# Optimization experiments

Measured on AMD Instinct MI355X. Metric: run time of the kernel, lower is better.

Reference implementation:

```python
import jax, jax.numpy as jnp
import numpy as np

NUM_EMB = 1024
EMB_DIM = 256
COMM_COST = 0.25
BETA = 0.25


def setup_inputs() -> dict:
    key = jax.random.key(0)
    k1, k2 = jax.random.split(key)
    x = jax.random.normal(k1, (16, EMB_DIM, 64, 64), dtype=jnp.float32)
    # nn.Embedding initialized uniform(-1/num_emb, 1/num_emb)
    emb_weight = jax.random.uniform(
        k2, (NUM_EMB, EMB_DIM), dtype=jnp.float32,
        minval=-1.0 / NUM_EMB, maxval=1.0 / NUM_EMB)
    return {"x": x, "emb_weight": emb_weight}


def reference(x, emb_weight):
    # x: [B, C, H, W] -> [B, H, W, C]
    xp = jnp.transpose(x, (0, 2, 3, 1))
    B, H, W, C = xp.shape
    flat = xp.reshape(-1, C)  # [N, C]
    # squared euclidean distances (argmin-equivalent to torch.cdist)
    d2 = (jnp.sum(flat * flat, axis=1, keepdims=True)
          - 2.0 * jnp.einsum('nc,kc->nk', flat, emb_weight)
          + jnp.sum(emb_weight * emb_weight, axis=1))  # [N, K]
    idx = jnp.argmin(d2, axis=1)  # [N]
    quantized = emb_weight[idx].reshape(B, H, W, C)
    e_latent_loss = jnp.mean((jax.lax.stop_gradient(quantized) - xp) ** 2) * BETA
    q_latent_loss = jnp.mean((quantized - jax.lax.stop_gradient(xp)) ** 2)
    c_loss = q_latent_loss + COMM_COST * e_latent_loss
    # straight-through estimator
    quant_st = xp + jax.lax.stop_gradient(quantized - xp)
    quant_out = jnp.transpose(quant_st, (0, 3, 1, 2))  # [B, C, H, W]
    return (c_loss, quant_out)
```

## Files before the change

### kernel.cpp

```cpp
#include <hip/hip_runtime.h>
#include <hip/hip_bf16.h>
#include <cstdint>
#include <cstddef>

#define EMB_K   1024
#define EMB_C   256
#define HWB     4096
#define NPIX    65536

typedef __bf16 bf16x8 __attribute__((ext_vector_type(8)));
typedef float  f32x4  __attribute__((ext_vector_type(4)));

__device__ __forceinline__ unsigned short bf16bits(float v) {
  __hip_bfloat16 h = __float2bfloat16(v);
  return __builtin_bit_cast(unsigned short, h);
}

__global__ void k_emb(const float* __restrict__ emb, unsigned short* __restrict__ emb_bf,
                      float* __restrict__ enorm, float* __restrict__ loss) {
  int k = blockIdx.x;
  int c = threadIdx.x;
  if (k == 0 && c == 0) *loss = 0.f;
  float v = emb[(size_t)k * EMB_C + c];
  emb_bf[(size_t)k * EMB_C + c] = bf16bits(v);
  float s = v * v;
  for (int m = 32; m; m >>= 1) s += __shfl_down(s, m, 64);
  __shared__ float red[4];
  int lane = c & 63, w = c >> 6;
  if (lane == 0) red[w] = s;
  __syncthreads();
  if (c == 0) enorm[k] = red[0] + red[1] + red[2] + red[3];
}

__global__ __launch_bounds__(512) void
k_tr(const float* __restrict__ x, unsigned short* __restrict__ A,
     float* __restrict__ xn_g) {
  __shared__ float xn_l[64];
  int t  = threadIdx.x;
  int n0 = blockIdx.x * 64;
  int b  = n0 >> 12, hw0 = n0 & 4095;
  int hwq = t & 15, c8 = t >> 4;
  if (t < 64) xn_l[t] = 0.f;
  __syncthreads();
  const float* xp = x + (size_t)b * (EMB_C * HWB) + hw0 + hwq * 4;
  float xn[4] = {0.f, 0.f, 0.f, 0.f};
  unsigned pk[4][4] = {};
#pragma unroll
  for (int j = 0; j < 8; ++j) {
    f32x4 v = *(const f32x4*)(xp + (size_t)(c8 * 8 + j) * HWB);
#pragma unroll
    for (int m = 0; m < 4; ++m) {
      xn[m] += v[m] * v[m];
      pk[m][j >> 1] |= (unsigned)bf16bits(v[m]) << ((j & 1) * 16);
    }
  }
  int s = c8 >> 2, quad = c8 & 3;
  uint4* A16 = (uint4*)A;
#pragma unroll
  for (int m = 0; m < 4; ++m) {
    int n  = n0 + hwq * 4 + m;
    int blk = n >> 8, nl = n & 255;
    int g = nl >> 6, i = (nl >> 4) & 3, lr = nl & 15;
    A16[(size_t)blk * 8192 + ((g * 4 + i) * 8 + s) * 64 + quad * 16 + lr]
        = *(const uint4*)pk[m];
    atomicAdd(&xn_l[hwq * 4 + m], xn[m]);
  }
  __syncthreads();
  if (t < 64) xn_g[n0 + t] = xn_l[t];
}

__device__ __forceinline__ void stage64(const unsigned short* __restrict__ rows,
                                        unsigned char* buf, int t) {
#pragma unroll
  for (int j = 0; j < 4; ++j) {
    int d = j * 512 + t;
    int r = d >> 5;
    int slot = d & 31;
    int c16 = ((slot >> 3) << 3) | ((slot & 7) ^ (r & 7));
    const unsigned short* src = rows + (size_t)r * EMB_C + c16 * 8;
    __builtin_amdgcn_global_load_lds(
        (const __attribute__((address_space(1))) void*)src,
        (__attribute__((address_space(3))) void*)(buf + (unsigned)(j * 8192 + (t >> 6) * 1024)),
        16, 0, 0);
  }
}

#define LDS_BYTES 137280

__global__ __launch_bounds__(512) void
k_main(const unsigned short* __restrict__ A, const unsigned short* __restrict__ embbf,
       const float* __restrict__ enorm, const float* __restrict__ xn_g,
       unsigned* __restrict__ keys_g, float* __restrict__ loss) {
  extern __shared__ char smem[];
  float*    cjl    = (float*)(smem + 131072);
  unsigned* keys_l = (unsigned*)(smem + 135168);
  float*    xn_l   = (float*)(smem + 136192);
  float*    red    = (float*)(smem + 137216);

  int n0 = blockIdx.x * 256;
  int t = threadIdx.x, w = t >> 6, lane = t & 63;
  int quad = lane >> 4, lr = lane & 15;
  int g  = w >> 1;
  int h2 = w & 1;

  stage64(embbf,               (unsigned char*)smem,         t);
  stage64(embbf + 64 * EMB_C,  (unsigned char*)smem + 32768, t);

  if (t < 256) { keys_l[t] = 0u; xn_l[t] = xn_g[n0 + t]; }
  for (int i = t; i < 1024; i += 512) cjl[i] = 0.375f - 0.5f * enorm[i];

  bf16x8 af[4][8];
  const uint4* Ab = (const uint4*)A + (size_t)blockIdx.x * 8192;
#pragma unroll
  for (int i = 0; i < 4; ++i)
#pragma unroll
    for (int s = 0; s < 8; ++s) {
      uint4 q = Ab[((g * 4 + i) * 8 + s) * 64 + lane];
      af[i][s] = __builtin_bit_cast(bf16x8, q);
    }
  __syncthreads();

  unsigned best[4][4] = {};
  for (int kt = 0; kt < 16; ++kt) {
    if (kt < 14)
      stage64(embbf + (size_t)(kt + 2) * 64 * EMB_C,
              (unsigned char*)smem + (((kt + 2) & 3) << 15), t);
    if (kt < 14)       asm volatile("s_waitcnt vmcnt(8)" ::: "memory");
    else if (kt == 14) asm volatile("s_waitcnt vmcnt(4)" ::: "memory");
    else               asm volatile("s_waitcnt vmcnt(0)" ::: "memory");
    __builtin_amdgcn_s_barrier();
    __builtin_amdgcn_sched_barrier(0);
    const unsigned char* srcB = (const unsigned char*)smem + ((kt & 3) << 15);
    float cj[2]; unsigned kp[2];
#pragma unroll
    for (int j = 0; j < 2; ++j) {
      int k = kt * 64 + h2 * 32 + j * 16 + lr;
      cj[j] = cjl[k];
      kp[j] = 1023u - (unsigned)k;
    }
    f32x4 acc[4][2] = {};
#pragma unroll
    for (int s = 0; s < 8; ++s) {
      int cc = s * 4 + quad;
      int pos = ((cc >> 3) << 3) | ((cc & 7) ^ (lr & 7));
      bf16x8 bf[2];
#pragma unroll
      for (int j = 0; j < 2; ++j)
        bf[j] = *(const bf16x8*)(srcB + (h2 * 32 + j * 16 + lr) * 512 + pos * 16);
#pragma unroll
      for (int i = 0; i < 4; ++i)
#pragma unroll
        for (int j = 0; j < 2; ++j)
          acc[i][j] = __builtin_amdgcn_mfma_f32_16x16x32_bf16(af[i][s], bf[j], acc[i][j], 0, 0, 0);
    }
#pragma unroll
    for (int i = 0; i < 4; ++i)
#pragma unroll
      for (int j = 0; j < 2; ++j)
#pragma unroll
        for (int r = 0; r < 4; ++r) {
          float f = acc[i][j][r] + cj[j];
          unsigned key = (__float_as_uint(f) & 0xFFFFFC00u) | kp[j];
          best[i][r] = best[i][r] > key ? best[i][r] : key;
        }
  }
  __syncthreads();

#pragma unroll
  for (int i = 0; i < 4; ++i)
#pragma unroll
    for (int r = 0; r < 4; ++r) {
      unsigned v = best[i][r];
#pragma unroll
      for (int m = 1; m < 16; m <<= 1) {
        unsigned o = (unsigned)__shfl_xor((int)v, m, 64);
        v = v > o ? v : o;
      }
      if (lr == 0) atomicMax(&keys_l[g * 64 + i * 16 + quad * 4 + r], v);
    }
  __syncthreads();

  if (t < 256) {
    unsigned key = keys_l[t];
    keys_g[n0 + t] = key;
    float fh = __uint_as_float(key & 0xFFFFFC00u);
    float lsum = xn_l[t] + 0.75f - 2.0f * fh;
    for (int m = 32; m; m >>= 1) lsum += __shfl_down(lsum, m, 64);
    if (lane == 0) red[w] = lsum;
  }
  __syncthreads();
  if (t == 0)
    atomicAdd(loss, red[0] + red[1] + red[2] + red[3]);
}

__global__ __launch_bounds__(256) void
k_out(const float* __restrict__ emb, const unsigned* __restrict__ keys_g,
      const float* __restrict__ loss, float* __restrict__ out) {
  __shared__ float tile[64 * 65];
  __shared__ int   idx_l[64];
  int e  = blockIdx.x;
  int nt = e >> 1, cH = e & 1;
  int n0 = nt * 64;
  int b  = n0 >> 12, hw0 = n0 & 4095;
  int t = threadIdx.x, w = t >> 6, lane = t & 63;
  if (e == 0 && t == 0)
    out[0] = 1.0625f * (*loss) / 16777216.0f;
  if (t < 64) idx_l[t] = 1023 - (int)(keys_g[n0 + t] & 1023u);
  __syncthreads();
  int nn = t >> 2, ch = t & 3;
  const float* er = emb + (size_t)idx_l[nn] * EMB_C + cH * 128;
  float* ob = out + 1 + (size_t)b * (EMB_C * HWB) + (size_t)cH * 128 * HWB + hw0;
  for (int p = 0; p < 2; ++p) {
    if (p) __syncthreads();
#pragma unroll
    for (int q = 0; q < 4; ++q) {
      f32x4 v = *(const f32x4*)(er + p * 64 + q * 16 + ch * 4);
#pragma unroll
      for (int m = 0; m < 4; ++m)
        tile[(q * 16 + ch * 4 + m) * 65 + nn] = v[m];
    }
    __syncthreads();
#pragma unroll
    for (int cc = 0; cc < 16; ++cc) {
      int cl = w * 16 + cc;
      ob[(size_t)(p * 64 + cl) * HWB + lane] = tile[cl * 65 + lane];
    }
  }
}

extern "C" void kernel_launch(void* const* d_in, const int* in_sizes, int n_in,
                              void* d_out, int out_size, void* d_ws, size_t ws_size,
                              hipStream_t stream) {
  const float* x   = (const float*)d_in[0];
  const float* emb = (const float*)d_in[1];
  float* out = (float*)d_out;
  char*  ws  = (char*)d_ws;

  unsigned short* emb_bf = (unsigned short*)ws;
  float*          enorm  = (float*)(ws + 524288);
  float*          loss   = (float*)(ws + 528384);
  float*          xn_g   = (float*)(ws + 532480);
  unsigned*       keys_g = (unsigned*)(ws + 794624);

  unsigned short* A = (unsigned short*)(out + 4);

  hipFuncSetAttribute((const void*)k_main,
                      hipFuncAttributeMaxDynamicSharedMemorySize, LDS_BYTES);

  k_emb <<<dim3(EMB_K),      dim3(EMB_C), 0,         stream>>>(emb, emb_bf, enorm, loss);
  k_tr  <<<dim3(NPIX / 64),  dim3(512),   0,         stream>>>(x, A, xn_g);
  k_main<<<dim3(NPIX / 256), dim3(512),   LDS_BYTES, stream>>>(A, emb_bf, enorm, xn_g,
                                                               keys_g, loss);
  k_out <<<dim3(NPIX / 32),  dim3(256),   0,         stream>>>(emb, keys_g, loss, out);
}
```

Before: 172.4 us.

## Halve codebook tile to 32 rows and stage transpose writes through LDS

The main distance kernel now streams the bf16 codebook in 32-row tiles instead of 64-row tiles. That halves LDS use from about 137KB to about 72KB, which could allow two blocks per CU, and halves the per-iteration accumulator registers. The cost is twice as many barrier-synchronised iterations and less B reuse per barrier. The transpose kernel now builds its packed A tile in swizzled shared memory and writes it out contiguously, replacing scattered global stores.

```diff
diff --git a/kernel.cpp b/kernel.cpp
--- a/kernel.cpp
+++ b/kernel.cpp
@@ -35,6 +35,7 @@
 __global__ __launch_bounds__(512) void
 k_tr(const float* __restrict__ x, unsigned short* __restrict__ A,
      float* __restrict__ xn_g) {
+  __shared__ uint4 tile[2048];
   __shared__ float xn_l[64];
   int t  = threadIdx.x;
   int n0 = blockIdx.x * 64;
@@ -55,24 +56,29 @@
     }
   }
   int s = c8 >> 2, quad = c8 & 3;
-  uint4* A16 = (uint4*)A;
 #pragma unroll
   for (int m = 0; m < 4; ++m) {
-    int n  = n0 + hwq * 4 + m;
-    int blk = n >> 8, nl = n & 255;
-    int g = nl >> 6, i = (nl >> 4) & 3, lr = nl & 15;
-    A16[(size_t)blk * 8192 + ((g * 4 + i) * 8 + s) * 64 + quad * 16 + lr]
-        = *(const uint4*)pk[m];
-    atomicAdd(&xn_l[hwq * 4 + m], xn[m]);
+    int nl = hwq * 4 + m;
+    int i = nl >> 4, lr = nl & 15;
+    int local = (i * 8 + s) * 64 + quad * 16 + lr;
+    tile[local ^ (quad << 1)] = *(const uint4*)pk[m];
+    atomicAdd(&xn_l[nl], xn[m]);
   }
   __syncthreads();
   if (t < 64) xn_g[n0 + t] = xn_l[t];
-}
-
-__device__ __forceinline__ void stage64(const unsigned short* __restrict__ rows,
+  int blk = n0 >> 8, g = (n0 >> 6) & 3;
+  uint4* dst = (uint4*)A + (size_t)blk * 8192 + g * 2048;
+#pragma unroll
+  for (int q = 0; q < 4; ++q) {
+    int d = q * 512 + t;
+    dst[d] = tile[d ^ (((d >> 4) & 3) << 1)];
+  }
+}
+
+__device__ __forceinline__ void stage32(const unsigned short* __restrict__ rows,
                                         unsigned char* buf, int t) {
 #pragma unroll
-  for (int j = 0; j < 4; ++j) {
+  for (int j = 0; j < 2; ++j) {
     int d = j * 512 + t;
     int r = d >> 5;
     int slot = d & 31;
@@ -85,17 +91,17 @@
   }
 }
 
-#define LDS_BYTES 137280
+#define LDS_BYTES 71744
 
 __global__ __launch_bounds__(512) void
 k_main(const unsigned short* __restrict__ A, const unsigned short* __restrict__ embbf,
        const float* __restrict__ enorm, const float* __restrict__ xn_g,
        unsigned* __restrict__ keys_g, float* __restrict__ loss) {
   extern __shared__ char smem[];
-  float*    cjl    = (float*)(smem + 131072);
-  unsigned* keys_l = (unsigned*)(smem + 135168);
-  float*    xn_l   = (float*)(smem + 136192);
-  float*    red    = (float*)(smem + 137216);
+  float*    cjl    = (float*)(smem + 65536);
+  unsigned* keys_l = (unsigned*)(smem + 69632);
+  float*    xn_l   = (float*)(smem + 70656);
+  float*    red    = (float*)(smem + 71680);
 
   int n0 = blockIdx.x * 256;
   int t = threadIdx.x, w = t >> 6, lane = t & 63;
@@ -103,8 +109,8 @@
   int g  = w >> 1;
   int h2 = w & 1;
 
-  stage64(embbf,               (unsigned char*)smem,         t);
-  stage64(embbf + 64 * EMB_C,  (unsigned char*)smem + 32768, t);
+  stage32(embbf,               (unsigned char*)smem,         t);
+  stage32(embbf + 32 * EMB_C,  (unsigned char*)smem + 16384, t);
 
   if (t < 256) { keys_l[t] = 0u; xn_l[t] = xn_g[n0 + t]; }
   for (int i = t; i < 1024; i += 512) cjl[i] = 0.375f - 0.5f * enorm[i];
@@ -121,48 +127,37 @@
   __syncthreads();
 
   unsigned best[4][4] = {};
-  for (int kt = 0; kt < 16; ++kt) {
-    if (kt < 14)
-      stage64(embbf + (size_t)(kt + 2) * 64 * EMB_C,
-              (unsigned char*)smem + (((kt + 2) & 3) << 15), t);
-    if (kt < 14)       asm volatile("s_waitcnt vmcnt(8)" ::: "memory");
-    else if (kt == 14) asm volatile("s_waitcnt vmcnt(4)" ::: "memory");
+  for (int kt = 0; kt < 32; ++kt) {
+    if (kt < 30)
+      stage32(embbf + (size_t)(kt + 2) * 32 * EMB_C,
+              (unsigned char*)smem + (((kt + 2) & 3) << 14), t);
+    if (kt < 30)       asm volatile("s_waitcnt vmcnt(4)" ::: "memory");
+    else if (kt == 30) asm volatile("s_waitcnt vmcnt(2)" ::: "memory");
     else               asm volatile("s_waitcnt vmcnt(0)" ::: "memory");
     __builtin_amdgcn_s_barrier();
     __builtin_amdgcn_sched_barrier(0);
-    const unsigned char* srcB = (const unsigned char*)smem + ((kt & 3) << 15);
-    float cj[2]; unsigned kp[2];
-#pragma unroll
-    for (int j = 0; j < 2; ++j) {
-      int k = kt * 64 + h2 * 32 + j * 16 + lr;
-      cj[j] = cjl[k];
-      kp[j] = 1023u - (unsigned)k;
-    }
-    f32x4 acc[4][2] = {};
+    const unsigned char* srcB = (const unsigned char*)smem + ((kt & 3) << 14);
+    int k = kt * 32 + h2 * 16 + lr;
+    float cj = cjl[k];
+    unsigned kp = 1023u - (unsigned)k;
+    f32x4 acc[4] = {};
 #pragma unroll
     for (int s = 0; s < 8; ++s) {
       int cc = s * 4 + quad;
       int pos = ((cc >> 3) << 3) | ((cc & 7) ^ (lr & 7));
-      bf16x8 bf[2];
-#pragma unroll
-      for (int j = 0; j < 2; ++j)
-        bf[j] = *(const bf16x8*)(srcB + (h2 * 32 + j * 16 + lr) * 512 + pos * 16);
+      bf16x8 bf = *(const bf16x8*)(srcB + (h2 * 16 + lr) * 512 + pos * 16);
 #pragma unroll
       for (int i = 0; i < 4; ++i)
-#pragma unroll
-        for (int j = 0; j < 2; ++j)
-          acc[i][j] = __builtin_amdgcn_mfma_f32_16x16x32_bf16(af[i][s], bf[j], acc[i][j], 0, 0, 0);
+        acc[i] = __builtin_amdgcn_mfma_f32_16x16x32_bf16(af[i][s], bf, acc[i], 0, 0, 0);
     }
 #pragma unroll
     for (int i = 0; i < 4; ++i)
 #pragma unroll
-      for (int j = 0; j < 2; ++j)
-#pragma unroll
-        for (int r = 0; r < 4; ++r) {
-          float f = acc[i][j][r] + cj[j];
-          unsigned key = (__float_as_uint(f) & 0xFFFFFC00u) | kp[j];
-          best[i][r] = best[i][r] > key ? best[i][r] : key;
-        }
+      for (int r = 0; r < 4; ++r) {
+        float f = acc[i][r] + cj;
+        unsigned key = (__float_as_uint(f) & 0xFFFFFC00u) | kp;
+        best[i][r] = best[i][r] > key ? best[i][r] : key;
+      }
   }
   __syncthreads();
 
```

After: 175.0 us. No clear change (+1.5%).
